# Kernel optimization log

Hardware: AMD Instinct MI355X
Metric: run time of the kernel (lower is better)

## Reference

```python
import jax, jax.numpy as jnp
import numpy as np

# ---------------- config (from ObjectDetector source) ----------------
B = 2; IMG = 224; STRIDE = 32; FH = IMG // STRIDE          # 7x7 feature map
C_FEAT = 1024
SIZES = (32., 64., 128., 256., 512.); RATIOS = (0.5, 1.0, 2.0)
A = len(SIZES) * len(RATIOS)                                # 15 anchors/loc
NA = FH * FH * A                                            # 735 anchors/img
PRE_NMS = min(1000, NA); POST_NMS = min(1000, NA)           # testing config
RPN_NMS_T = 0.7; RPN_MIN_SIZE = 1e-3
NUM_CLASSES = 37
ROI_OUT = 7; ROI_SR = 2; ROI_SCALE = 1.0 / STRIDE
REP = 1024
SCORE_T = 0.05; DET_NMS_T = 0.5; DETS_PER_IMG = 100
CAND_K = 2048            # candidate cap before final batched NMS
MIN_SIZE_DET = 1e-2
BBOX_CLIP = float(np.log(1000.0 / 16.0))


def make_anchors():
    scales = np.array(SIZES, np.float32); ratios = np.array(RATIOS, np.float32)
    h_r = np.sqrt(ratios); w_r = 1.0 / h_r
    ws = (w_r[:, None] * scales[None, :]).reshape(-1)
    hs = (h_r[:, None] * scales[None, :]).reshape(-1)
    base = np.round(np.stack([-ws, -hs, ws, hs], 1) / 2.0)   # [A,4]
    sy, sx = np.meshgrid(np.arange(FH) * STRIDE, np.arange(FH) * STRIDE, indexing='ij')
    shifts = np.stack([sx.reshape(-1), sy.reshape(-1), sx.reshape(-1), sy.reshape(-1)], 1).astype(np.float32)
    return jnp.asarray((shifts[:, None, :] + base[None, :, :]).reshape(-1, 4))  # [NA,4] (H,W,A)


def conv(x, w, b, stride=1, pad=0):
    y = jax.lax.conv_general_dilated(x, w, (stride, stride), [(pad, pad)] * 2,
                                     dimension_numbers=('NCHW', 'OIHW', 'NCHW'))
    return y + b[None, :, None, None]


def decode_boxes(deltas, boxes, weights):
    wx, wy, ww, wh = weights
    w = boxes[..., 2] - boxes[..., 0]; h = boxes[..., 3] - boxes[..., 1]
    cx = boxes[..., 0] + 0.5 * w; cy = boxes[..., 1] + 0.5 * h
    dx = deltas[..., 0] / wx; dy = deltas[..., 1] / wy
    dw = jnp.minimum(deltas[..., 2] / ww, BBOX_CLIP)
    dh = jnp.minimum(deltas[..., 3] / wh, BBOX_CLIP)
    pcx = dx * w + cx; pcy = dy * h + cy
    pw = jnp.exp(dw) * w; ph = jnp.exp(dh) * h
    return jnp.stack([pcx - 0.5 * pw, pcy - 0.5 * ph, pcx + 0.5 * pw, pcy + 0.5 * ph], -1)


def clip_boxes(b):
    x = jnp.clip(b[..., 0::2], 0.0, float(IMG)); y = jnp.clip(b[..., 1::2], 0.0, float(IMG))
    return jnp.stack([x[..., 0], y[..., 0], x[..., 1], y[..., 1]], -1)


def box_iou(a, b):
    area_a = (a[:, 2] - a[:, 0]) * (a[:, 3] - a[:, 1])
    area_b = (b[:, 2] - b[:, 0]) * (b[:, 3] - b[:, 1])
    lt = jnp.maximum(a[:, None, :2], b[None, :, :2])
    rb = jnp.minimum(a[:, None, 2:], b[None, :, 2:])
    wh = jnp.clip(rb - lt, 0.0, None)
    inter = wh[..., 0] * wh[..., 1]
    return inter / jnp.maximum(area_a[:, None] + area_b[None, :] - inter, 1e-9)


def nms_keep(boxes, scores, thresh):
    """Greedy NMS; returns keep mask in original order (fixed shapes)."""
    n = boxes.shape[0]
    order = jnp.argsort(-scores)
    iou = box_iou(*(jax.lax.stop_gradient(boxes[order]),) * 2)
    idx = jnp.arange(n)
    def body(i, keep):
        sup = (iou[i] > thresh) & (idx > i) & keep[i]
        return keep & ~sup
    keep_sorted = jax.lax.fori_loop(0, n, body, jnp.ones(n, bool))
    return jnp.zeros(n, bool).at[order].set(keep_sorted)


def rpn_filter_one(obj_logits, deltas, anchors):
    # obj_logits [NA], deltas [NA,4] (detached, as in torchvision RPN)
    top_v, top_i = jax.lax.top_k(obj_logits, PRE_NMS)
    boxes = clip_boxes(decode_boxes(deltas[top_i], anchors[top_i], (1., 1., 1., 1.)))
    prob = jax.nn.sigmoid(top_v)
    ws = boxes[:, 2] - boxes[:, 0]; hs = boxes[:, 3] - boxes[:, 1]
    prob = jnp.where((ws >= RPN_MIN_SIZE) & (hs >= RPN_MIN_SIZE), prob, -1.0)
    prob = jnp.where(nms_keep(boxes, prob, RPN_NMS_T), prob, -1.0)
    sv, si = jax.lax.top_k(prob, POST_NMS)
    return boxes[si], sv > 0.0


def bilinear(f_hwc, ys, xs):
    # torchvision roi_align bilinear sampling; f_hwc [H,W,C], ys/xs [R,O]
    H, W, _ = f_hwc.shape
    vy = (ys >= -1.0) & (ys <= H); vx = (xs >= -1.0) & (xs <= W)
    y = jnp.clip(ys, 0.0, None); x = jnp.clip(xs, 0.0, None)
    y0 = jnp.minimum(jnp.floor(y).astype(jnp.int32), H - 1)
    x0 = jnp.minimum(jnp.floor(x).astype(jnp.int32), W - 1)
    y1 = jnp.minimum(y0 + 1, H - 1); x1 = jnp.minimum(x0 + 1, W - 1)
    y = jnp.where(y0 == H - 1, y0.astype(y.dtype), y)
    x = jnp.where(x0 == W - 1, x0.astype(x.dtype), x)
    ly = y - y0; lx = x - x0; hy = 1.0 - ly; hx = 1.0 - lx
    g = lambda yi, xi: f_hwc[yi[:, :, None], xi[:, None, :]]   # [R,O,O,C]
    val = ((hy[:, :, None] * hx[:, None, :])[..., None] * g(y0, x0)
         + (hy[:, :, None] * lx[:, None, :])[..., None] * g(y0, x1)
         + (ly[:, :, None] * hx[:, None, :])[..., None] * g(y1, x0)
         + (ly[:, :, None] * lx[:, None, :])[..., None] * g(y1, x1))
    return val * (vy[:, :, None] & vx[:, None, :])[..., None]


def roi_align_one(feat_chw, rois):
    # feat [C,H,W], rois [R,4] -> [R,C,7,7]; output_size=7, sampling_ratio=2, scale=1/32
    f = jnp.transpose(feat_chw, (1, 2, 0))
    x1 = rois[:, 0] * ROI_SCALE; y1 = rois[:, 1] * ROI_SCALE
    rw = jnp.maximum(rois[:, 2] * ROI_SCALE - x1, 1.0)
    rh = jnp.maximum(rois[:, 3] * ROI_SCALE - y1, 1.0)
    bw = rw / ROI_OUT; bh = rh / ROI_OUT
    grid = jnp.arange(ROI_OUT, dtype=jnp.float32)
    acc = 0.0
    for iy in range(ROI_SR):
        ys = y1[:, None] + (grid[None, :] + (iy + 0.5) / ROI_SR) * bh[:, None]
        for ix in range(ROI_SR):
            xs = x1[:, None] + (grid[None, :] + (ix + 0.5) / ROI_SR) * bw[:, None]
            acc = acc + bilinear(f, ys, xs)
    return jnp.transpose(acc / (ROI_SR * ROI_SR), (0, 3, 1, 2))


def postprocess_one(logits, box_deltas, proposals, roi_valid):
    R = logits.shape[0]
    scores = jax.nn.softmax(logits, -1)
    boxes = clip_boxes(decode_boxes(box_deltas.reshape(R, NUM_CLASSES, 4),
                                    proposals[:, None, :], (10., 10., 5., 5.)))
    boxes = boxes[:, 1:, :].reshape(-1, 4)       # drop background class
    scores = jnp.where(roi_valid[:, None], scores[:, 1:], 0.0).reshape(-1)
    labels = jnp.broadcast_to(jnp.arange(1, NUM_CLASSES)[None, :], (R, NUM_CLASSES - 1)).reshape(-1)
    ws = boxes[:, 2] - boxes[:, 0]; hs = boxes[:, 3] - boxes[:, 1]
    ok = (ws >= MIN_SIZE_DET) & (hs >= MIN_SIZE_DET) & (scores > SCORE_T)
    cs, ci = jax.lax.top_k(jnp.where(ok, scores, -1.0), CAND_K)
    cb = boxes[ci]; cl = labels[ci]
    off = cl.astype(cb.dtype) * (IMG + 1.0)      # batched (per-class) NMS trick
    keep = nms_keep(cb + off[:, None], cs, DET_NMS_T)
    tv, ti = jax.lax.top_k(jnp.where(keep, cs, -1.0), DETS_PER_IMG)
    valid = tv > 0.0
    out_boxes = jnp.where(valid[:, None], cb[ti], 0.0)
    out_scores = jnp.where(valid, tv, 0.0)
    out_labels = jnp.where(valid, cl[ti], 0).astype(out_boxes.dtype)
    return jnp.concatenate([out_boxes, out_scores[:, None], out_labels[:, None]], -1)  # [100,6]


def forward(images, params, anchors):
    (bb_w, bb_b, rpn_w, rpn_b, cls_w, cls_b, reg_w, reg_b,
     fc1_w, fc1_b, fc2_w, fc2_b, clsp_w, clsp_b, boxp_w, boxp_b) = params
    Bn = images.shape[0]
    feats = jax.nn.relu(conv(images, bb_w, bb_b, stride=STRIDE))        # [B,1024,7,7]
    t = jax.nn.relu(conv(feats, rpn_w, rpn_b, stride=1, pad=1))
    obj = jnp.transpose(conv(t, cls_w, cls_b), (0, 2, 3, 1)).reshape(Bn, -1)            # [B,NA]
    reg = jnp.transpose(conv(t, reg_w, reg_b).reshape(Bn, A, 4, FH, FH),
                        (0, 3, 4, 1, 2)).reshape(Bn, -1, 4)                              # [B,NA,4]
    obj_d = jax.lax.stop_gradient(obj); reg_d = jax.lax.stop_gradient(reg)  # RPN detaches
    proposals, roi_valid = jax.vmap(lambda o, d: rpn_filter_one(o, d, anchors))(obj_d, reg_d)
    pooled = jax.vmap(roi_align_one)(feats, proposals)                  # [B,R,1024,7,7]
    x = pooled.reshape(Bn * POST_NMS, -1)
    x = jax.nn.relu(x @ fc1_w.T + fc1_b)
    x = jax.nn.relu(x @ fc2_w.T + fc2_b)
    logits = (x @ clsp_w.T + clsp_b).reshape(Bn, POST_NMS, NUM_CLASSES)
    bdelt = (x @ boxp_w.T + boxp_b).reshape(Bn, POST_NMS, NUM_CLASSES * 4)
    return jax.vmap(postprocess_one)(logits, bdelt, proposals, roi_valid)  # [B,100,6]


def setup_inputs() -> dict:
    key = jax.random.key(0)
    ks = jax.random.split(key, 10)
    w = lambda k, shape, s=0.02: jax.random.normal(k, shape, jnp.float32) * s
    return {
        'images': jax.random.uniform(ks[0], (B, 1, IMG, IMG), jnp.float32),
        'bb_w': w(ks[1], (C_FEAT, 1, STRIDE, STRIDE)), 'bb_b': jnp.zeros((C_FEAT,), jnp.float32),
        'rpn_w': w(ks[2], (C_FEAT, C_FEAT, 3, 3)), 'rpn_b': jnp.zeros((C_FEAT,), jnp.float32),
        'cls_w': w(ks[3], (A, C_FEAT, 1, 1)), 'cls_b': jnp.zeros((A,), jnp.float32),
        'reg_w': w(ks[4], (4 * A, C_FEAT, 1, 1)), 'reg_b': jnp.zeros((4 * A,), jnp.float32),
        'fc1_w': w(ks[5], (REP, C_FEAT * ROI_OUT * ROI_OUT), 0.005), 'fc1_b': jnp.zeros((REP,), jnp.float32),
        'fc2_w': w(ks[6], (REP, REP)), 'fc2_b': jnp.zeros((REP,), jnp.float32),
        'clsp_w': w(ks[7], (NUM_CLASSES, REP)), 'clsp_b': jnp.zeros((NUM_CLASSES,), jnp.float32),
        'boxp_w': w(ks[8], (NUM_CLASSES * 4, REP)), 'boxp_b': jnp.zeros((NUM_CLASSES * 4,), jnp.float32),
    }


def reference(images, bb_w, bb_b, rpn_w, rpn_b, cls_w, cls_b, reg_w, reg_b,
              fc1_w, fc1_b, fc2_w, fc2_b, clsp_w, clsp_b, boxp_w, boxp_b):
    anchors = make_anchors()
    params = (bb_w, bb_b, rpn_w, rpn_b, cls_w, cls_b, reg_w, reg_b,
              fc1_w, fc1_b, fc2_w, fc2_b, clsp_w, clsp_b, boxp_w, boxp_b)
    return forward(images, params, anchors)
```

## Files before the change

### kernel.cpp

```cpp
#include <hip/hip_runtime.h>
#include <math.h>

#define NANCH 735
#define NCAND 26460
#define NCANDP 26624
#define BBCLIP 4.135166556742356f
#define KF1 4864
#define KHALF 2432

typedef short bf16x8 __attribute__((ext_vector_type(8)));
typedef float f32x4 __attribute__((ext_vector_type(4)));

__device__ __forceinline__ unsigned short f2b(float f) {
  unsigned int u = __float_as_uint(f);
  unsigned int r = (u >> 16) & 1u;
  u += 0x7fffu + r;
  return (unsigned short)(u >> 16);
}

__device__ __forceinline__ void anchor_of(int i, float* o) {
  int pos = i / 15, a = i % 15;
  int iy = pos / 7, ix = pos % 7;
  int rr = a / 5, sc = a % 5;
  double ratio = (rr == 0) ? 0.5 : (rr == 1 ? 1.0 : 2.0);
  double scale = (double)(32 << sc);
  double hr = sqrt(ratio), wr = 1.0 / hr;
  double wsz = wr * scale, hsz = hr * scale;
  float bx1 = (float)rint(-wsz * 0.5), by1 = (float)rint(-hsz * 0.5);
  float bx2 = (float)rint(wsz * 0.5),  by2 = (float)rint(hsz * 0.5);
  float sx = (float)(ix * 32), sy = (float)(iy * 32);
  o[0] = sx + bx1; o[1] = sy + by1; o[2] = sx + bx2; o[3] = sy + by2;
}

__device__ __forceinline__ bool before_(float va, int ia, float vb, int ib) {
  return (va > vb) || (va == vb && ia < ib);
}

template<int NTOT, int NTH>
__device__ void bitonic_sort_sh(float* v, int* id) {
  const int t = threadIdx.x;
  for (int k = 2; k <= NTOT; k <<= 1) {
    for (int j = k >> 1; j > 0; j >>= 1) {
      for (int s = t; s < NTOT; s += NTH) {
        int p = s ^ j;
        if (p > s) {
          float v1 = v[s], v2 = v[p];
          int i1 = id[s], i2 = id[p];
          bool up = ((s & k) == 0);
          if (before_(v2, i2, v1, i1) == up) {
            v[s] = v2; id[s] = i2; v[p] = v1; id[p] = i1;
          }
        }
      }
      __syncthreads();
    }
  }
}

template<int NTOT, int NTH>
__device__ void bitonic_merge_sh(float* v, int* id) {
  const int t = threadIdx.x;
  for (int j = NTOT >> 1; j > 0; j >>= 1) {
    for (int s = t; s < NTOT; s += NTH) {
      int p = s ^ j;
      if (p > s) {
        float v1 = v[s], v2 = v[p];
        int i1 = id[s], i2 = id[p];
        if (before_(v2, i2, v1, i1)) {
          v[s] = v2; id[s] = i2; v[p] = v1; id[p] = i1;
        }
      }
    }
    __syncthreads();
  }
}

__global__ void k_im2col_bb(const float* __restrict__ images, unsigned short* __restrict__ patch) {
  int i = blockIdx.x * 256 + threadIdx.x;
  if (i >= 98 * 1024) return;
  int rowi = i >> 10, k = i & 1023;
  int b = rowi / 49, pos = rowi % 49;
  int oy = pos / 7, ox = pos % 7;
  int ky = k >> 5, kx = k & 31;
  patch[i] = f2b(images[((size_t)b * 224 + oy * 32 + ky) * 224 + ox * 32 + kx]);
}

__global__ void k_im2col_rpn(const unsigned short* __restrict__ bbh,
                             unsigned short* __restrict__ im2) {
  int i = blockIdx.x * 256 + threadIdx.x;
  if (i >= 98 * 9216) return;
  int rowi = i / 9216, k = i % 9216;
  int b = rowi / 49, pos = rowi % 49;
  int oy = pos / 7, ox = pos % 7;
  int ic = k / 9, kk = k % 9;
  int ky = kk / 3, kx = kk % 3;
  int y = oy + ky - 1, x = ox + kx - 1;
  unsigned short v = 0;
  if ((unsigned)y < 7u && (unsigned)x < 7u)
    v = bbh[((size_t)(b * 49 + y * 7 + x)) * 1024 + ic];
  im2[i] = v;
}

__global__ __launch_bounds__(256) void k_gemm_bf16(
    const unsigned short* __restrict__ A, int lda, int M,
    const unsigned short* __restrict__ B, int ldb,
    float* __restrict__ P, int N, int Kchunk,
    const int* __restrict__ nvalid)
{
  __shared__ __attribute__((aligned(16))) unsigned short As[2][128][40];
  __shared__ __attribute__((aligned(16))) unsigned short Bs[2][128][40];
  const int G = gridDim.x * gridDim.y * gridDim.z;
  int lid = blockIdx.x + gridDim.x * (blockIdx.y + gridDim.y * blockIdx.z);
  lid = (lid & 7) * (G >> 3) + (lid >> 3);
  const int bx = lid % gridDim.x;
  const int rest = lid / gridDim.x;
  const int by = rest % gridDim.y, bz = rest / gridDim.y;
  const int m0 = bx * 128, n0 = by * 128;
  if (nvalid) {
    int nv0 = nvalid[0], nv1 = nvalid[1];
    bool ok = (m0 < nv0) || ((m0 + 128 > NANCH) && (m0 < NANCH + nv1));
    if (!ok) return;
  }
  const int t = threadIdx.x;
  const int lane = t & 63, wid = t >> 6;
  const int wm = (wid >> 1) * 64, wn = (wid & 1) * 64;
  const size_t k0 = (size_t)bz * Kchunk;
  f32x4 acc[4][4];
#pragma unroll
  for (int i = 0; i < 4; ++i)
#pragma unroll
    for (int j = 0; j < 4; ++j) acc[i][j] = (f32x4){0.f, 0.f, 0.f, 0.f};
  const int r0 = t >> 2, c0 = (t & 3) * 8;
  const int fr = lane & 15, fk = (lane >> 4) * 8;
  const int gmA0 = m0 + r0, gmA1 = m0 + r0 + 64;
  const bool vA0 = gmA0 < M, vA1 = gmA1 < M;
  const unsigned short* pA0 = A + (size_t)gmA0 * lda + k0 + c0;
  const unsigned short* pA1 = A + (size_t)gmA1 * lda + k0 + c0;
  const unsigned short* pB0 = B + (size_t)(n0 + r0) * ldb + k0 + c0;
  const unsigned short* pB1 = B + (size_t)(n0 + r0 + 64) * ldb + k0 + c0;
  bf16x8 rA0 = {}, rA1 = {}, rB0, rB1;
  if (vA0) rA0 = *(const bf16x8*)pA0;
  if (vA1) rA1 = *(const bf16x8*)pA1;
  rB0 = *(const bf16x8*)pB0;
  rB1 = *(const bf16x8*)pB1;
  const int nt = Kchunk >> 5;
  int cur = 0;
  for (int it = 0; it < nt; ++it) {
    *(bf16x8*)&As[cur][r0][c0] = rA0;
    *(bf16x8*)&As[cur][r0 + 64][c0] = rA1;
    *(bf16x8*)&Bs[cur][r0][c0] = rB0;
    *(bf16x8*)&Bs[cur][r0 + 64][c0] = rB1;
    __syncthreads();
    if (it + 1 < nt) {
      size_t ofs = (size_t)(it + 1) * 32;
      rA0 = vA0 ? *(const bf16x8*)(pA0 + ofs) : (bf16x8){};
      rA1 = vA1 ? *(const bf16x8*)(pA1 + ofs) : (bf16x8){};
      rB0 = *(const bf16x8*)(pB0 + ofs);
      rB1 = *(const bf16x8*)(pB1 + ofs);
    }
    bf16x8 af[4], bg[4];
#pragma unroll
    for (int i = 0; i < 4; ++i) af[i] = *(const bf16x8*)&As[cur][wm + i * 16 + fr][fk];
#pragma unroll
    for (int j = 0; j < 4; ++j) bg[j] = *(const bf16x8*)&Bs[cur][wn + j * 16 + fr][fk];
#pragma unroll
    for (int i = 0; i < 4; ++i)
#pragma unroll
      for (int j = 0; j < 4; ++j)
        acc[i][j] = __builtin_amdgcn_mfma_f32_16x16x32_bf16(af[i], bg[j], acc[i][j], 0, 0, 0);
    cur ^= 1;
  }
  float* Pp = P + (size_t)bz * M * N;
#pragma unroll
  for (int i = 0; i < 4; ++i) {
#pragma unroll
    for (int r = 0; r < 4; ++r) {
      int gm = m0 + wm + i * 16 + (lane >> 4) * 4 + r;
      if (gm < M) {
#pragma unroll
        for (int j = 0; j < 4; ++j)
          Pp[(size_t)gm * N + n0 + wn + j * 16 + (lane & 15)] = acc[i][j][r];
      }
    }
  }
}

__global__ __launch_bounds__(256) void k_gemm_mb(
    const unsigned short* __restrict__ A,
    const unsigned short* __restrict__ W1p,
    unsigned short* __restrict__ Bmat)
{
  __shared__ __attribute__((aligned(16))) unsigned short As[2][128][40];
  __shared__ __attribute__((aligned(16))) unsigned short Bs[2][128][40];
  __shared__ unsigned short tile[98][130];
  const int G = gridDim.x * gridDim.y * gridDim.z;
  int lid = blockIdx.x + gridDim.x * (blockIdx.y + gridDim.y * blockIdx.z);
  lid = (lid & 7) * (G >> 3) + (lid >> 3);
  const int rest = lid;
  const int by = rest % gridDim.y, p = rest / gridDim.y;
  const int n0 = by * 128;
  const int M = 98;
  const unsigned short* B = W1p + (size_t)p * 1048576;
  const int t = threadIdx.x;
  const int lane = t & 63, wid = t >> 6;
  const int wm = (wid >> 1) * 64, wn = (wid & 1) * 64;
  f32x4 acc[4][4];
#pragma unroll
  for (int i = 0; i < 4; ++i)
#pragma unroll
    for (int j = 0; j < 4; ++j) acc[i][j] = (f32x4){0.f, 0.f, 0.f, 0.f};
  const int r0 = t >> 2, c0 = (t & 3) * 8;
  const int fr = lane & 15, fk = (lane >> 4) * 8;
  int gA0 = r0; if (gA0 >= M) gA0 = M - 1;
  int gA1 = r0 + 64; if (gA1 >= M) gA1 = M - 1;
  const unsigned short* pA0 = A + (size_t)gA0 * 1024 + c0;
  const unsigned short* pA1 = A + (size_t)gA1 * 1024 + c0;
  const unsigned short* pB0 = B + (size_t)(n0 + r0) * 1024 + c0;
  const unsigned short* pB1 = B + (size_t)(n0 + r0 + 64) * 1024 + c0;
  bf16x8 rA0 = *(const bf16x8*)pA0;
  bf16x8 rA1 = *(const bf16x8*)pA1;
  bf16x8 rB0 = *(const bf16x8*)pB0;
  bf16x8 rB1 = *(const bf16x8*)pB1;
  const int nt = 1024 >> 5;
  int cur = 0;
  for (int it = 0; it < nt; ++it) {
    *(bf16x8*)&As[cur][r0][c0] = rA0;
    *(bf16x8*)&As[cur][r0 + 64][c0] = rA1;
    *(bf16x8*)&Bs[cur][r0][c0] = rB0;
    *(bf16x8*)&Bs[cur][r0 + 64][c0] = rB1;
    __syncthreads();
    if (it + 1 < nt) {
      size_t ofs = (size_t)(it + 1) * 32;
      rA0 = *(const bf16x8*)(pA0 + ofs);
      rA1 = *(const bf16x8*)(pA1 + ofs);
      rB0 = *(const bf16x8*)(pB0 + ofs);
      rB1 = *(const bf16x8*)(pB1 + ofs);
    }
    bf16x8 af[4], bg[4];
#pragma unroll
    for (int i = 0; i < 4; ++i) af[i] = *(const bf16x8*)&As[cur][wm + i * 16 + fr][fk];
#pragma unroll
    for (int j = 0; j < 4; ++j) bg[j] = *(const bf16x8*)&Bs[cur][wn + j * 16 + fr][fk];
#pragma unroll
    for (int i = 0; i < 4; ++i)
#pragma unroll
      for (int j = 0; j < 4; ++j)
        acc[i][j] = __builtin_amdgcn_mfma_f32_16x16x32_bf16(af[i], bg[j], acc[i][j], 0, 0, 0);
    cur ^= 1;
  }
  __syncthreads();
#pragma unroll
  for (int i = 0; i < 4; ++i) {
#pragma unroll
    for (int r = 0; r < 4; ++r) {
      int gm = wm + i * 16 + (lane >> 4) * 4 + r;
      if (gm < M) {
#pragma unroll
        for (int j = 0; j < 4; ++j)
          tile[gm][wn + j * 16 + (lane & 15)] = f2b(acc[i][j][r]);
      }
    }
  }
  __syncthreads();
  {
    int nl = t >> 1, b2 = t & 1;
    unsigned short* dst = Bmat + (size_t)(n0 + nl) * KF1 + b2 * KHALF + p * 49;
    for (int qq = 0; qq < 49; ++qq) dst[qq] = tile[b2 * 49 + qq][nl];
  }
  if (p == 0) {
    for (int j2 = t; j2 < 128 * 62; j2 += 256) {
      int nl = j2 / 62, e = j2 % 62;
      int bb = e >= 31 ? 1 : 0;
      int col = bb * KHALF + 2401 + (e - bb * 31);
      Bmat[(size_t)(n0 + nl) * KF1 + col] = 0;
    }
  }
}

__global__ __launch_bounds__(256) void k_gbuild(const float* __restrict__ props,
                                                unsigned short* __restrict__ Gmat)
{
#pragma clang fp contract(off)
  int rg = blockIdx.x;
  int b = rg / NANCH;
  __shared__ float g[KF1];
  int t = threadIdx.x;
  for (int j = t; j < KF1; j += 256) g[j] = 0.f;
  __syncthreads();
  if (t < 49) {
    const float* roi = props + (size_t)rg * 4;
    int p = t, oy = p / 7, ox = p % 7;
    float x1 = roi[0] * 0.03125f, y1 = roi[1] * 0.03125f;
    float rw = fmaxf(roi[2] * 0.03125f - x1, 1.f);
    float rh = fmaxf(roi[3] * 0.03125f - y1, 1.f);
    float bw = rw / 7.f, bh = rh / 7.f;
    float* gb = g + b * KHALF + p * 49;
    for (int iy = 0; iy < 2; ++iy) {
      for (int ix = 0; ix < 2; ++ix) {
        float ys = y1 + ((float)oy + ((float)iy + 0.5f) * 0.5f) * bh;
        float xs = x1 + ((float)ox + ((float)ix + 0.5f) * 0.5f) * bw;
        bool vy = (ys >= -1.f) && (ys <= 7.f);
        bool vx = (xs >= -1.f) && (xs <= 7.f);
        float yc = fmaxf(ys, 0.f), xc = fmaxf(xs, 0.f);
        int y0 = min((int)floorf(yc), 6), x0 = min((int)floorf(xc), 6);
        int y1i = min(y0 + 1, 6), x1i = min(x0 + 1, 6);
        if (y0 == 6) yc = 6.f;
        if (x0 == 6) xc = 6.f;
        float ly = yc - (float)y0, lx = xc - (float)x0;
        float hy = 1.f - ly, hx = 1.f - lx;
        float vm = (vy && vx) ? 0.25f : 0.f;
        gb[y0 * 7 + x0]   += hy * hx * vm;
        gb[y0 * 7 + x1i]  += hy * lx * vm;
        gb[y1i * 7 + x0]  += ly * hx * vm;
        gb[y1i * 7 + x1i] += ly * lx * vm;
      }
    }
  }
  __syncthreads();
  unsigned short* Gr = Gmat + (size_t)rg * KF1;
  for (int j = t; j < KF1; j += 256) Gr[j] = f2b(g[j]);
}

__global__ void k_reduce(const float* __restrict__ P, float* __restrict__ dst,
                         unsigned short* __restrict__ dst16,
                         int S, int M, int N, const float* __restrict__ bias, int flags)
{
  size_t i = (size_t)blockIdx.x * 256 + threadIdx.x;
  size_t tot = (size_t)M * N;
  if (i >= tot) return;
  float v = (flags & 1) ? 0.f : dst[i];
  for (int s = 0; s < S; ++s) v += P[(size_t)s * tot + i];
  if (flags & 2) v += bias[i % (size_t)N];
  if (flags & 4) v = fmaxf(v, 0.f);
  if (!(flags & 16)) dst[i] = v;
  if (flags & 8) dst16[i] = f2b(v);
}

__global__ void k_f2b3(const float* __restrict__ s1, unsigned short* __restrict__ d1,
                       const float* __restrict__ s2, unsigned short* __restrict__ d2,
                       const float* __restrict__ s3, unsigned short* __restrict__ d3,
                       const float* __restrict__ cw, const float* __restrict__ bw,
                       unsigned short* __restrict__ d4)
{
  int i = (blockIdx.x * 256 + threadIdx.x) * 4;
  const float* s; unsigned short* d; int off;
  if (i < 1048576) { s = s1; d = d1; off = i; }
  else if (i < 2097152) { s = s2; d = d2; off = i - 1048576; }
  else if (i < 11534336) { s = s3; d = d3; off = i - 2097152; }
  else if (i < 11796480) {
    int off4 = i - 11534336;
    int row = off4 >> 10, col = off4 & 1023;
    ushort4 o;
    if (row < 37) {
      float4 v = *(const float4*)(cw + (size_t)row * 1024 + col);
      o.x = f2b(v.x); o.y = f2b(v.y); o.z = f2b(v.z); o.w = f2b(v.w);
    } else if (row < 185) {
      float4 v = *(const float4*)(bw + (size_t)(row - 37) * 1024 + col);
      o.x = f2b(v.x); o.y = f2b(v.y); o.z = f2b(v.z); o.w = f2b(v.w);
    } else {
      o.x = 0; o.y = 0; o.z = 0; o.w = 0;
    }
    *(ushort4*)(d4 + off4) = o;
    return;
  }
  else return;
  float4 v = *(const float4*)(s + off);
  ushort4 o;
  o.x = f2b(v.x); o.y = f2b(v.y); o.z = f2b(v.z); o.w = f2b(v.w);
  *(ushort4*)(d + off) = o;
}

__global__ __launch_bounds__(256) void k_w1perm2(const float* __restrict__ w,
                                                 unsigned short* __restrict__ o)
{
  __shared__ unsigned short tile[128 * 50];
  const int n = blockIdx.x, ct = blockIdx.y;
  const float* src = w + (size_t)n * 50176 + (size_t)ct * 128 * 49;
  const int t = threadIdx.x;
  for (int i = t; i < 6272; i += 256) {
    int cl = i / 49, p = i % 49;
    tile[cl * 50 + p] = f2b(src[i]);
  }
  __syncthreads();
  for (int j = t; j < 6272; j += 256) {
    int p = j >> 7, cl = j & 127;
    o[((size_t)p * 1024 + n) * 1024 + (size_t)ct * 128 + cl] = tile[cl * 50 + p];
  }
}

__global__ __launch_bounds__(256) void k_rpn_head(
    const float* __restrict__ tmn, const float* __restrict__ cls_w,
    const float* __restrict__ cls_b, const float* __restrict__ reg_w,
    const float* __restrict__ reg_b, float* __restrict__ obj, float* __restrict__ reg)
{
  int blk = blockIdx.x;
  __shared__ float col[1024];
  const float* row = tmn + (size_t)blk * 1024;
  for (int i = threadIdx.x; i < 1024; i += 256) col[i] = row[i];
  __syncthreads();
  int b = blk / 49, pos = blk % 49;
  for (int o = threadIdx.x; o < 75; o += 256) {
    const float* w = (o < 15) ? (cls_w + (size_t)o * 1024) : (reg_w + (size_t)(o - 15) * 1024);
    float s = 0.f;
    for (int k = 0; k < 1024; ++k) s = fmaf(col[k], w[k], s);
    if (o < 15) {
      obj[(size_t)b * NANCH + pos * 15 + o] = s + cls_b[o];
    } else {
      int c = o - 15, a = c >> 2, d = c & 3;
      reg[((size_t)b * NANCH + pos * 15 + a) * 4 + d] = s + reg_b[c];
    }
  }
}

__global__ __launch_bounds__(1024) void k_rpn_prep(
    const float* __restrict__ obj, const float* __restrict__ reg,
    float* __restrict__ bxp, float* __restrict__ pnms)
{
#pragma clang fp contract(off)
  const int b = blockIdx.x, t = threadIdx.x;
  __shared__ float sval[1024];
  __shared__ float vo1[1024];
  __shared__ int o1a[1024];
  __shared__ int wtv[16];
  __shared__ int wti[16];
  sval[t] = (t < NANCH) ? obj[(size_t)b * NANCH + t] : -INFINITY;
  __syncthreads();
  {
    float v = sval[t];
    int rank = 0;
    for (int j = 0; j < NANCH; ++j) {
      float u = sval[j];
      rank += (u > v) || (u == v && j < t);
    }
    if (t < NANCH) { vo1[rank] = v; o1a[rank] = t; }
  }
  __syncthreads();
  float x1 = 0.f, y1 = 0.f, x2 = 0.f, y2 = 0.f, prob = -1.f;
  bool flag = false;
  if (t < NANCH) {
    int ai = o1a[t];
    const float* d = reg + ((size_t)b * NANCH + ai) * 4;
    float an[4];
    anchor_of(ai, an);
    float aw = an[2] - an[0], ah = an[3] - an[1];
    float acx = an[0] + 0.5f * aw, acy = an[1] + 0.5f * ah;
    float dw = fminf(d[2], BBCLIP), dh = fminf(d[3], BBCLIP);
    float pcx = d[0] * aw + acx, pcy = d[1] * ah + acy;
    float pw = expf(dw) * aw, ph = expf(dh) * ah;
    x1 = pcx - 0.5f * pw; y1 = pcy - 0.5f * ph;
    x2 = pcx + 0.5f * pw; y2 = pcy + 0.5f * ph;
    x1 = fminf(fmaxf(x1, 0.f), 224.f);
    y1 = fminf(fmaxf(y1, 0.f), 224.f);
    x2 = fminf(fmaxf(x2, 0.f), 224.f);
    y2 = fminf(fmaxf(y2, 0.f), 224.f);
    flag = (x2 - x1 >= 1e-3f) && (y2 - y1 >= 1e-3f);
    prob = 1.f / (1.f + expf(-vo1[t]));
  }
  bool iflag = (t < NANCH) && !flag;
  unsigned long long balv = __ballot(flag);
  unsigned long long bali = __ballot(iflag);
  int lane = t & 63, w = t >> 6;
  if (lane == 0) { wtv[w] = __popcll(balv); wti[w] = __popcll(bali); }
  __syncthreads();
  int nval = 0, basev = 0, basei = 0;
  for (int k = 0; k < 16; ++k) {
    int cv = wtv[k], ci = wti[k];
    nval += cv;
    if (k < w) { basev += cv; basei += ci; }
  }
  if (t < NANCH) {
    unsigned long long lm = (1ull << lane) - 1;
    int pos = flag ? (basev + __popcll(balv & lm))
                   : (nval + basei + __popcll(bali & lm));
    float* o = bxp + ((size_t)b * NANCH + pos) * 4;
    o[0] = x1; o[1] = y1; o[2] = x2; o[3] = y2;
    pnms[(size_t)b * NANCH + pos] = flag ? prob : -1.f;
  }
}

__global__ __launch_bounds__(256) void k_rpn_mask(
    const float* __restrict__ bxp, unsigned long long* __restrict__ rmask)
{
#pragma clang fp contract(off)
  int blk = blockIdx.x;
  int b = blk / 35;
  int row = (blk % 35) * 21 + (int)(threadIdx.x / 12);
  int w = threadIdx.x % 12;
  if (threadIdx.x >= 252 || row >= NANCH) return;
  const float* a = bxp + ((size_t)b * NANCH + row) * 4;
  float a0 = a[0], a1 = a[1], a2 = a[2], a3 = a[3];
  float aarea = (a2 - a0) * (a3 - a1);
  int l0 = w * 64;
  int l1 = (l0 + 64 < NANCH) ? l0 + 64 : NANCH;
  int ls = (l0 > row + 1) ? l0 : row + 1;
  unsigned long long bits = 0ull;
  for (int l = ls; l < l1; ++l) {
    const float* q = bxp + ((size_t)b * NANCH + l) * 4;
    float b0 = q[0], b1 = q[1], b2 = q[2], b3 = q[3];
    float barea = (b2 - b0) * (b3 - b1);
    float ix1 = fmaxf(a0, b0), iy1 = fmaxf(a1, b1);
    float ix2 = fminf(a2, b2), iy2 = fminf(a3, b3);
    float iw = fmaxf(ix2 - ix1, 0.f), ih = fmaxf(iy2 - iy1, 0.f);
    float inter = iw * ih;
    float iou = inter / fmaxf(aarea + barea - inter, 1e-9f);
    if (iou > 0.7f) bits |= 1ull << (l & 63);
  }
  rmask[((size_t)b * NANCH + row) * 12 + w] = bits;
}

__global__ __launch_bounds__(1024) void k_rpn_fin(
    const float* __restrict__ bxp, const float* __restrict__ pnms,
    const unsigned long long* __restrict__ rmask,
    float* __restrict__ props, int* __restrict__ meta)
{
  const int b = blockIdx.x, t = threadIdx.x;
  __shared__ unsigned long long smask[NANCH * 12];
  __shared__ float sp[1024];
  __shared__ unsigned long long keepw[12];
  __shared__ int wtot[16];
  for (int i = t; i < NANCH * 12; i += 1024)
    smask[i] = rmask[(size_t)b * NANCH * 12 + i];
  sp[t] = (t < NANCH) ? pnms[(size_t)b * NANCH + t] : -1.f;
  __syncthreads();
  if (t < 64) {
    unsigned long long kl = (t < 12) ? ~0ull : 0ull;
    for (int i = 0; i < NANCH; ++i) {
      unsigned long long kw = __shfl(kl, i >> 6);
      unsigned long long m = (t < 12) ? smask[i * 12 + t] : 0ull;
      bool on = (kw >> (i & 63)) & 1ull;
      kl &= on ? ~m : ~0ull;
    }
    if (t < 12) keepw[t] = kl;
  }
  __syncthreads();
  bool flag = false;
  if (t < NANCH) {
    bool kp = (keepw[t >> 6] >> (t & 63)) & 1ull;
    flag = kp && (sp[t] > 0.f);
  }
  unsigned long long bal = __ballot(flag);
  int lane = t & 63, w = t >> 6;
  if (lane == 0) wtot[w] = __popcll(bal);
  __syncthreads();
  int base = 0, tot = 0;
  for (int k = 0; k < 16; ++k) { int c = wtot[k]; if (k < w) base += c; tot += c; }
  if (flag) {
    int pos = base + __popcll(bal & ((1ull << lane) - 1));
    const float* src = bxp + ((size_t)b * NANCH + t) * 4;
    float* o = props + ((size_t)b * NANCH + pos) * 4;
    o[0] = src[0]; o[1] = src[1]; o[2] = src[2]; o[3] = src[3];
  }
  if (t == 0) meta[b] = tot;
}

__global__ void k_cand(const float* __restrict__ P, const float* __restrict__ cb_,
                       const float* __restrict__ bb_, const float* __restrict__ props,
                       const int* __restrict__ meta,
                       float* __restrict__ cscore, float* __restrict__ cbox)
{
#pragma clang fp contract(off)
  int rg = blockIdx.x * blockDim.x + threadIdx.x;
  if (rg >= 2 * NANCH) return;
  int b = rg / NANCH, r = rg % NANCH;
  float* cs = cscore + (size_t)b * NCANDP;
  float* cbx = cbox + (size_t)b * NCANDP * 4;
  int base = r * 36;
  if (r >= meta[b]) {
    for (int j = 0; j < 36; ++j) {
      cs[base + j] = -1.f;
      float* q = cbx + (size_t)(base + j) * 4;
      q[0] = 0.f; q[1] = 0.f; q[2] = 0.f; q[3] = 0.f;
    }
    return;
  }
  const float* p0 = P + (size_t)rg * 256;
  const float* p1 = P + 1470ull * 256 + (size_t)rg * 256;
  float lg[37];
  for (int c = 0; c < 37; ++c) lg[c] = p0[c] + p1[c] + cb_[c];
  float mx = lg[0];
  for (int c = 1; c < 37; ++c) mx = fmaxf(mx, lg[c]);
  float sum = 0.f;
  for (int c = 0; c < 37; ++c) sum += expf(lg[c] - mx);
  const float* roi = props + (size_t)rg * 4;
  float rw = roi[2] - roi[0], rh = roi[3] - roi[1];
  float rcx = roi[0] + 0.5f * rw, rcy = roi[1] + 0.5f * rh;
  for (int c = 1; c < 37; ++c) {
    float d0 = p0[37 + c * 4]     + p1[37 + c * 4]     + bb_[c * 4];
    float d1 = p0[37 + c * 4 + 1] + p1[37 + c * 4 + 1] + bb_[c * 4 + 1];
    float d2 = p0[37 + c * 4 + 2] + p1[37 + c * 4 + 2] + bb_[c * 4 + 2];
    float d3 = p0[37 + c * 4 + 3] + p1[37 + c * 4 + 3] + bb_[c * 4 + 3];
    float dx = d0 / 10.f, dy = d1 / 10.f;
    float dw = fminf(d2 / 5.f, BBCLIP), dh = fminf(d3 / 5.f, BBCLIP);
    float pcx = dx * rw + rcx, pcy = dy * rh + rcy;
    float pw = expf(dw) * rw, ph = expf(dh) * rh;
    float x1 = pcx - 0.5f * pw, y1 = pcy - 0.5f * ph;
    float x2 = pcx + 0.5f * pw, y2 = pcy + 0.5f * ph;
    x1 = fminf(fmaxf(x1, 0.f), 224.f);
    y1 = fminf(fmaxf(y1, 0.f), 224.f);
    x2 = fminf(fmaxf(x2, 0.f), 224.f);
    y2 = fminf(fmaxf(y2, 0.f), 224.f);
    float sc = expf(lg[c] - mx) / sum;
    bool ok = ((x2 - x1) >= 1e-2f) && ((y2 - y1) >= 1e-2f) && (sc > 0.05f);
    cs[base + c - 1] = ok ? sc : -1.f;
    float* q = cbx + (size_t)(base + c - 1) * 4;
    q[0] = x1; q[1] = y1; q[2] = x2; q[3] = y2;
  }
}

__global__ __launch_bounds__(1024) void k_top2048(
    const float* __restrict__ cscore,
    float* __restrict__ sel_score, int* __restrict__ sel_cidx,
    int* __restrict__ meta)
{
  const int b = blockIdx.x, t = threadIdx.x;
  __shared__ float Lv[2048]; __shared__ int Li[2048];
  __shared__ float Cv[2048]; __shared__ int Ci[2048];
  __shared__ int cnt;
  const float* cs = cscore + (size_t)b * NCANDP;
  if (t == 0) cnt = 0;
  __syncthreads();
  for (int gi = t; gi < NCAND; gi += 1024) {
    float v = cs[gi];
    if (v > 0.f) {
      int p = atomicAdd(&cnt, 1);
      if (p < 2048) { Cv[p] = v; Ci[p] = gi; }
    }
  }
  __syncthreads();
  int npos = cnt;
  if (npos <= 2048) {
    for (int h = 0; h < 2; ++h) {
      int p = h * 1024 + t;
      if (p < npos) {
        float v = Cv[p]; int id = Ci[p];
        int rank = 0;
        for (int j = 0; j < npos; ++j) {
          float u = Cv[j]; int ju = Ci[j];
          rank += (u > v) || (u == v && ju < id);
        }
        sel_score[b * 2048 + rank] = v;
        sel_cidx[b * 2048 + rank] = id;
      }
      if (p >= npos && p < 2048) {
        sel_score[b * 2048 + p] = -1.f;
        sel_cidx[b * 2048 + p] = 0;
      }
    }
    if (t == 0) meta[2 + b] = npos;
    return;
  }
  for (int chunk = 0; chunk < 13; ++chunk) {
    for (int s = t; s < 2048; s += 1024) {
      int gi = chunk * 2048 + s;
      Cv[s] = (gi < NCAND) ? cs[gi] : -INFINITY;
      Ci[s] = gi;
    }
    __syncthreads();
    bitonic_sort_sh<2048, 1024>(Cv, Ci);
    if (chunk == 0) {
      for (int s = t; s < 2048; s += 1024) { Lv[s] = Cv[s]; Li[s] = Ci[s]; }
      __syncthreads();
    } else {
      for (int s = t; s < 2048; s += 1024) {
        float cv = Cv[2047 - s]; int ci = Ci[2047 - s];
        if (before_(cv, ci, Lv[s], Li[s])) { Lv[s] = cv; Li[s] = ci; }
      }
      __syncthreads();
      bitonic_merge_sh<2048, 1024>(Lv, Li);
    }
  }
  for (int s = t; s < 2048; s += 1024) {
    sel_score[b * 2048 + s] = Lv[s];
    sel_cidx[b * 2048 + s] = Li[s];
  }
  if (t == 0) meta[2 + b] = 2048;
}

__global__ void k_detmask(const int* __restrict__ sel_cidx,
                          const float* __restrict__ cbox,
                          const int* __restrict__ meta,
                          unsigned long long* __restrict__ dmask)
{
#pragma clang fp contract(off)
  int blk = blockIdx.x;
  int b = blk >> 8, row0 = (blk & 255) * 8;
  int npos = meta[2 + b];
  if (row0 >= npos) return;
  int t = threadIdx.x;
  int i = row0 + (t >> 5), w = t & 31;
  if (i >= npos) return;
  int ci = sel_cidx[b * 2048 + i];
  const float* bp = cbox + ((size_t)b * NCANDP + ci) * 4;
  float off = (float)(ci % 36 + 1) * 225.f;
  float a0 = bp[0] + off, a1 = bp[1] + off, a2 = bp[2] + off, a3 = bp[3] + off;
  float aarea = (a2 - a0) * (a3 - a1);
  unsigned long long bits = 0ull;
  int l0 = w * 64;
  int l1 = (l0 + 64 < npos) ? l0 + 64 : npos;
  int ls = (l0 > i + 1) ? l0 : i + 1;
  for (int l = ls; l < l1; ++l) {
    int cl = sel_cidx[b * 2048 + l];
    const float* q = cbox + ((size_t)b * NCANDP + cl) * 4;
    float o2 = (float)(cl % 36 + 1) * 225.f;
    float b0 = q[0] + o2, b1 = q[1] + o2, b2 = q[2] + o2, b3 = q[3] + o2;
    float barea = (b2 - b0) * (b3 - b1);
    float ix1 = fmaxf(a0, b0), iy1 = fmaxf(a1, b1);
    float ix2 = fminf(a2, b2), iy2 = fminf(a3, b3);
    float iw = fmaxf(ix2 - ix1, 0.f), ih = fmaxf(iy2 - iy1, 0.f);
    float inter = iw * ih;
    float iou = inter / fmaxf(aarea + barea - inter, 1e-9f);
    if (iou > 0.5f) bits |= 1ull << (l & 63);
  }
  dmask[((size_t)b * 2048 + i) * 32 + w] = bits;
}

__global__ __launch_bounds__(1024) void k_final(
    const float* __restrict__ sel_score, const int* __restrict__ sel_cidx,
    const float* __restrict__ cbox, const unsigned long long* __restrict__ dmask,
    const int* __restrict__ meta, float* __restrict__ out)
{
  const int b = blockIdx.x, t = threadIdx.x;
  __shared__ unsigned long long keepw[32];
  __shared__ float sv[2048];
  __shared__ float kv[2048]; __shared__ int ks[2048];
  __shared__ int wtot[32];
  int npos = meta[2 + b];
  for (int h = 0; h < 2; ++h) {
    int s = h * 1024 + t;
    sv[s] = sel_score[b * 2048 + s];
  }
  __syncthreads();
  if (t < 64) {
    unsigned long long kl = (t < 32) ? ~0ull : 0ull;
    for (int i = 0; i < npos; ++i) {
      unsigned long long kw = __shfl(kl, i >> 6);
      unsigned long long m = (t < 32) ? dmask[((size_t)b * 2048 + i) * 32 + t] : 0ull;
      bool on = (kw >> (i & 63)) & 1ull;
      kl &= on ? ~m : ~0ull;
    }
    if (t < 32) keepw[t] = kl;
  }
  __syncthreads();
  const int lane = t & 63, w = t >> 6;
  int s0 = t;
  bool f0 = ((keepw[s0 >> 6] >> (s0 & 63)) & 1ull) && (sv[s0] > 0.f);
  unsigned long long bal0 = __ballot(f0);
  if (lane == 0) wtot[w] = __popcll(bal0);
  int s1 = 1024 + t;
  bool f1 = ((keepw[s1 >> 6] >> (s1 & 63)) & 1ull) && (sv[s1] > 0.f);
  unsigned long long bal1 = __ballot(f1);
  if (lane == 0) wtot[16 + w] = __popcll(bal1);
  __syncthreads();
  int nk = 0, base0 = 0, base1 = 0;
  for (int k = 0; k < 32; ++k) {
    int c = wtot[k];
    if (k < w) base0 += c;
    if (k < 16 + w) base1 += c;
    nk += c;
  }
  int p0 = -1, p1 = -1;
  if (f0) { p0 = base0 + __popcll(bal0 & ((1ull << lane) - 1)); kv[p0] = sv[s0]; ks[p0] = s0; }
  if (f1) { p1 = base1 + __popcll(bal1 & ((1ull << lane) - 1)); kv[p1] = sv[s1]; ks[p1] = s1; }
  __syncthreads();
  if (f0) {
    float v = sv[s0]; int rank = 0;
    for (int j = 0; j < nk; ++j) { float u = kv[j]; int ju = ks[j]; rank += (u > v) || (u == v && ju < s0); }
    if (rank < 100) {
      int ci = sel_cidx[b * 2048 + s0];
      const float* bp = cbox + ((size_t)b * NCANDP + ci) * 4;
      float* o = out + ((size_t)b * 100 + rank) * 6;
      o[0] = bp[0]; o[1] = bp[1]; o[2] = bp[2]; o[3] = bp[3];
      o[4] = v; o[5] = (float)(ci % 36 + 1);
    }
  }
  if (f1) {
    float v = sv[s1]; int rank = 0;
    for (int j = 0; j < nk; ++j) { float u = kv[j]; int ju = ks[j]; rank += (u > v) || (u == v && ju < s1); }
    if (rank < 100) {
      int ci = sel_cidx[b * 2048 + s1];
      const float* bp = cbox + ((size_t)b * NCANDP + ci) * 4;
      float* o = out + ((size_t)b * 100 + rank) * 6;
      o[0] = bp[0]; o[1] = bp[1]; o[2] = bp[2]; o[3] = bp[3];
      o[4] = v; o[5] = (float)(ci % 36 + 1);
    }
  }
  if (t < 100 && t >= nk) {
    float* o = out + ((size_t)b * 100 + t) * 6;
    o[0] = 0.f; o[1] = 0.f; o[2] = 0.f; o[3] = 0.f; o[4] = 0.f; o[5] = 0.f;
  }
}

extern "C" void kernel_launch(void* const* d_in, const int* in_sizes, int n_in,
                              void* d_out, int out_size, void* d_ws, size_t ws_size,
                              hipStream_t stream)
{
  (void)in_sizes; (void)n_in; (void)out_size; (void)ws_size;
  const float* images = (const float*)d_in[0];
  const float* bb_w   = (const float*)d_in[1];
  const float* bb_b   = (const float*)d_in[2];
  const float* rpn_w  = (const float*)d_in[3];
  const float* rpn_b  = (const float*)d_in[4];
  const float* cls_w  = (const float*)d_in[5];
  const float* cls_b  = (const float*)d_in[6];
  const float* reg_w  = (const float*)d_in[7];
  const float* reg_b  = (const float*)d_in[8];
  const float* fc1_w  = (const float*)d_in[9];
  const float* fc1_b  = (const float*)d_in[10];
  const float* fc2_w  = (const float*)d_in[11];
  const float* fc2_b  = (const float*)d_in[12];
  const float* clsp_w = (const float*)d_in[13];
  const float* clsp_b = (const float*)d_in[14];
  const float* boxp_w = (const float*)d_in[15];
  const float* boxp_b = (const float*)d_in[16];
  float* out = (float*)d_out;
  char* ws = (char*)d_ws;

  size_t off = 0;
  auto alloc = [&](size_t bytes) -> size_t {
    size_t o = off; off = (off + bytes + 255) & ~(size_t)255; return o;
  };
  size_t o_patch = alloc(98ull * 1024 * 2);
  size_t o_bbC   = alloc(98ull * 1024 * 4);
  size_t o_bbh   = alloc(98ull * 1024 * 2);
  size_t o_t     = alloc(98ull * 1024 * 4);
  size_t o_im2   = alloc(98ull * 9216 * 2);
  size_t o_obj   = alloc(1470ull * 4);
  size_t o_reg   = alloc(1470ull * 16);
  size_t o_props = alloc(1470ull * 16);
  size_t o_bxp   = alloc(1470ull * 16);
  size_t o_pnms  = alloc(1470ull * 4);
  size_t o_rm    = alloc(1470ull * 12 * 8);
  size_t o_meta  = alloc(256);
  size_t o_y1    = alloc(1470ull * 1024 * 4);
  size_t o_y2    = alloc(1470ull * 1024 * 4);
  size_t o_cs    = alloc(2ull * NCANDP * 4);
  size_t o_cb    = alloc(2ull * NCANDP * 16);
  size_t o_ss    = alloc(2ull * 2048 * 4);
  size_t o_sc    = alloc(2ull * 2048 * 4);
  size_t o_dm    = alloc(2ull * 2048 * 32 * 8);
  size_t o_w0b   = alloc(1048576ull * 2);
  size_t o_w3b   = alloc(9437184ull * 2);
  size_t o_w1p   = alloc(51380224ull * 2);
  size_t o_bmat  = alloc(1024ull * KF1 * 2);
  size_t o_gmat  = alloc(1470ull * KF1 * 2);
  size_t o_w2b   = alloc(1048576ull * 2);
  size_t o_hwb   = alloc(256ull * 1024 * 2);
  size_t o_y1b   = alloc(1470ull * 1024 * 2);
  size_t o_y2b   = alloc(1470ull * 1024 * 2);
  size_t o_P     = alloc(32ull * 98 * 1024 * 4 > 4ull * 1470 * 1024 * 4
                         ? 32ull * 98 * 1024 * 4 : 4ull * 1470 * 1024 * 4);

  unsigned short* patchb = (unsigned short*)(ws + o_patch);
  float* bbC   = (float*)(ws + o_bbC);
  unsigned short* bbh = (unsigned short*)(ws + o_bbh);
  float* tb    = (float*)(ws + o_t);
  unsigned short* im2b = (unsigned short*)(ws + o_im2);
  float* objb  = (float*)(ws + o_obj);
  float* regb  = (float*)(ws + o_reg);
  float* props = (float*)(ws + o_props);
  float* bxp   = (float*)(ws + o_bxp);
  float* pnms  = (float*)(ws + o_pnms);
  unsigned long long* rmb = (unsigned long long*)(ws + o_rm);
  int*   meta  = (int*)(ws + o_meta);
  float* y1    = (float*)(ws + o_y1);
  float* csb   = (float*)(ws + o_cs);
  float* cbb   = (float*)(ws + o_cb);
  float* ssb   = (float*)(ws + o_ss);
  int*   scb   = (int*)(ws + o_sc);
  unsigned long long* dmb = (unsigned long long*)(ws + o_dm);
  unsigned short* w0b = (unsigned short*)(ws + o_w0b);
  unsigned short* w3b = (unsigned short*)(ws + o_w3b);
  unsigned short* w1p = (unsigned short*)(ws + o_w1p);
  unsigned short* bmat = (unsigned short*)(ws + o_bmat);
  unsigned short* gmat = (unsigned short*)(ws + o_gmat);
  unsigned short* w2b = (unsigned short*)(ws + o_w2b);
  unsigned short* hwb = (unsigned short*)(ws + o_hwb);
  unsigned short* y1b = (unsigned short*)(ws + o_y1b);
  unsigned short* y2b = (unsigned short*)(ws + o_y2b);
  float* Pb    = (float*)(ws + o_P);

  k_w1perm2<<<dim3(1024, 8), 256, 0, stream>>>(fc1_w, w1p);
  k_f2b3<<<11520, 256, 0, stream>>>(fc2_w, w2b, bb_w, w0b, rpn_w, w3b, clsp_w, boxp_w, hwb);
  k_im2col_bb<<<392, 256, 0, stream>>>(images, patchb);
  k_gemm_bf16<<<dim3(1, 8, 8), 256, 0, stream>>>(patchb, 1024, 98, w0b, 1024, Pb, 1024, 128, nullptr);
  k_reduce<<<392, 256, 0, stream>>>(Pb, bbC, bbh, 8, 98, 1024, bb_b, 31);
  k_gemm_mb<<<dim3(1, 8, 49), 256, 0, stream>>>(bbh, w1p, bmat);
  k_im2col_rpn<<<3528, 256, 0, stream>>>(bbh, im2b);
  k_gemm_bf16<<<dim3(1, 8, 32), 256, 0, stream>>>(im2b, 9216, 98, w3b, 9216, Pb, 1024, 288, nullptr);
  k_reduce<<<392, 256, 0, stream>>>(Pb, tb, nullptr, 32, 98, 1024, rpn_b, 7);
  k_rpn_head<<<98, 256, 0, stream>>>(tb, cls_w, cls_b, reg_w, reg_b, objb, regb);
  k_rpn_prep<<<2, 1024, 0, stream>>>(objb, regb, bxp, pnms);
  k_rpn_mask<<<70, 256, 0, stream>>>(bxp, rmb);
  k_rpn_fin<<<2, 1024, 0, stream>>>(bxp, pnms, rmb, props, meta);
  k_gbuild<<<1470, 256, 0, stream>>>(props, gmat);
  k_gemm_bf16<<<dim3(12, 8, 4), 256, 0, stream>>>(gmat, KF1, 1470, bmat, KF1, Pb, 1024, 1216, meta);
  k_reduce<<<5880, 256, 0, stream>>>(Pb, y1, y1b, 4, 1470, 1024, fc1_b, 31);
  k_gemm_bf16<<<dim3(12, 8, 2), 256, 0, stream>>>(y1b, 1024, 1470, w2b, 1024, Pb, 1024, 512, meta);
  k_reduce<<<5880, 256, 0, stream>>>(Pb, y1, y2b, 2, 1470, 1024, fc2_b, 31);
  k_gemm_bf16<<<dim3(12, 2, 2), 256, 0, stream>>>(y2b, 1024, 1470, hwb, 1024, Pb, 256, 512, meta);
  k_cand<<<6, 256, 0, stream>>>(Pb, clsp_b, boxp_b, props, meta, csb, cbb);
  k_top2048<<<2, 1024, 0, stream>>>(csb, ssb, scb, meta);
  k_detmask<<<512, 256, 0, stream>>>(scb, cbb, meta, dmb);
  k_final<<<2, 1024, 0, stream>>>(ssb, scb, cbb, dmb, meta, out);
}
```

Baseline: 455.1 us.

## Split fc1 ROI GEMM per image to skip the zero half of K

Each image's ROIs are padded to 768 rows so that every 128-row tile belongs to a single image. The per-image gather matrix now holds only that image's K half (2432 columns), and the GEMM shifts the B pointer by image. This halves the K work and gather-matrix traffic of the fc1 GEMM, since the other image's half was all zeros, and it halves the split-K partials to reduce. The cost is some padded rows (1536 vs 1470), a changed row indexing in the downstream kernels, and a new lower clamp on the bilinear indices.

```diff
diff --git a/kernel.cpp b/kernel.cpp
--- a/kernel.cpp
+++ b/kernel.cpp
@@ -7,6 +7,8 @@
 #define BBCLIP 4.135166556742356f
 #define KF1 4864
 #define KHALF 2432
+#define MROW 768
+#define MTOT 1536
 
 typedef short bf16x8 __attribute__((ext_vector_type(8)));
 typedef float f32x4 __attribute__((ext_vector_type(4)));
@@ -105,7 +107,7 @@
     const unsigned short* __restrict__ A, int lda, int M,
     const unsigned short* __restrict__ B, int ldb,
     float* __restrict__ P, int N, int Kchunk,
-    const int* __restrict__ nvalid)
+    const int* __restrict__ nvalid, int Msplit, int boff)
 {
   __shared__ __attribute__((aligned(16))) unsigned short As[2][128][40];
   __shared__ __attribute__((aligned(16))) unsigned short Bs[2][128][40];
@@ -117,9 +119,10 @@
   const int by = rest % gridDim.y, bz = rest / gridDim.y;
   const int m0 = bx * 128, n0 = by * 128;
   if (nvalid) {
-    int nv0 = nvalid[0], nv1 = nvalid[1];
-    bool ok = (m0 < nv0) || ((m0 + 128 > NANCH) && (m0 < NANCH + nv1));
-    if (!ok) return;
+    int img = (Msplit && m0 >= Msplit) ? 1 : 0;
+    int lm = m0 - img * Msplit;
+    if (lm >= nvalid[img]) return;
+    B += (size_t)img * boff;
   }
   const int t = threadIdx.x;
   const int lane = t & 63, wid = t >> 6;
@@ -282,19 +285,20 @@
 {
 #pragma clang fp contract(off)
   int rg = blockIdx.x;
-  int b = rg / NANCH;
-  __shared__ float g[KF1];
+  int b = rg / MROW, r = rg % MROW;
+  __shared__ float g[KHALF];
   int t = threadIdx.x;
-  for (int j = t; j < KF1; j += 256) g[j] = 0.f;
+  for (int j = t; j < KHALF; j += 256) g[j] = 0.f;
   __syncthreads();
   if (t < 49) {
-    const float* roi = props + (size_t)rg * 4;
+    int pr = b * NANCH + r; if (pr > 2 * NANCH - 1) pr = 2 * NANCH - 1;
+    const float* roi = props + (size_t)pr * 4;
     int p = t, oy = p / 7, ox = p % 7;
     float x1 = roi[0] * 0.03125f, y1 = roi[1] * 0.03125f;
     float rw = fmaxf(roi[2] * 0.03125f - x1, 1.f);
     float rh = fmaxf(roi[3] * 0.03125f - y1, 1.f);
     float bw = rw / 7.f, bh = rh / 7.f;
-    float* gb = g + b * KHALF + p * 49;
+    float* gb = g + p * 49;
     for (int iy = 0; iy < 2; ++iy) {
       for (int ix = 0; ix < 2; ++ix) {
         float ys = y1 + ((float)oy + ((float)iy + 0.5f) * 0.5f) * bh;
@@ -302,7 +306,7 @@
         bool vy = (ys >= -1.f) && (ys <= 7.f);
         bool vx = (xs >= -1.f) && (xs <= 7.f);
         float yc = fmaxf(ys, 0.f), xc = fmaxf(xs, 0.f);
-        int y0 = min((int)floorf(yc), 6), x0 = min((int)floorf(xc), 6);
+        int y0 = min(max((int)floorf(yc), 0), 6), x0 = min(max((int)floorf(xc), 0), 6);
         int y1i = min(y0 + 1, 6), x1i = min(x0 + 1, 6);
         if (y0 == 6) yc = 6.f;
         if (x0 == 6) xc = 6.f;
@@ -317,8 +321,8 @@
     }
   }
   __syncthreads();
-  unsigned short* Gr = Gmat + (size_t)rg * KF1;
-  for (int j = t; j < KF1; j += 256) Gr[j] = f2b(g[j]);
+  unsigned short* Gr = Gmat + (size_t)rg * KHALF;
+  for (int j = t; j < KHALF; j += 256) Gr[j] = f2b(g[j]);
 }
 
 __global__ void k_reduce(const float* __restrict__ P, float* __restrict__ dst,
@@ -573,8 +577,9 @@
     }
     return;
   }
-  const float* p0 = P + (size_t)rg * 256;
-  const float* p1 = P + 1470ull * 256 + (size_t)rg * 256;
+  int row = b * MROW + r;
+  const float* p0 = P + (size_t)row * 256;
+  const float* p1 = P + (size_t)MTOT * 256 + (size_t)row * 256;
   float lg[37];
   for (int c = 0; c < 37; ++c) lg[c] = p0[c] + p1[c] + cb_[c];
   float mx = lg[0];
@@ -831,8 +836,7 @@
   size_t o_pnms  = alloc(1470ull * 4);
   size_t o_rm    = alloc(1470ull * 12 * 8);
   size_t o_meta  = alloc(256);
-  size_t o_y1    = alloc(1470ull * 1024 * 4);
-  size_t o_y2    = alloc(1470ull * 1024 * 4);
+  size_t o_y1    = alloc((size_t)MTOT * 1024 * 4);
   size_t o_cs    = alloc(2ull * NCANDP * 4);
   size_t o_cb    = alloc(2ull * NCANDP * 16);
   size_t o_ss    = alloc(2ull * 2048 * 4);
@@ -842,13 +846,13 @@
   size_t o_w3b   = alloc(9437184ull * 2);
   size_t o_w1p   = alloc(51380224ull * 2);
   size_t o_bmat  = alloc(1024ull * KF1 * 2);
-  size_t o_gmat  = alloc(1470ull * KF1 * 2);
+  size_t o_gmat  = alloc((size_t)MTOT * KHALF * 2);
   size_t o_w2b   = alloc(1048576ull * 2);
   size_t o_hwb   = alloc(256ull * 1024 * 2);
-  size_t o_y1b   = alloc(1470ull * 1024 * 2);
-  size_t o_y2b   = alloc(1470ull * 1024 * 2);
-  size_t o_P     = alloc(32ull * 98 * 1024 * 4 > 4ull * 1470 * 1024 * 4
-                         ? 32ull * 98 * 1024 * 4 : 4ull * 1470 * 1024 * 4);
+  size_t o_y1b   = alloc((size_t)MTOT * 1024 * 2);
+  size_t o_y2b   = alloc((size_t)MTOT * 1024 * 2);
+  size_t o_P     = alloc(32ull * 98 * 1024 * 4 > 2ull * MTOT * 1024 * 4
+                         ? 32ull * 98 * 1024 * 4 : 2ull * MTOT * 1024 * 4);
 
   unsigned short* patchb = (unsigned short*)(ws + o_patch);
   float* bbC   = (float*)(ws + o_bbC);
@@ -882,22 +886,22 @@
   k_w1perm2<<<dim3(1024, 8), 256, 0, stream>>>(fc1_w, w1p);
   k_f2b3<<<11520, 256, 0, stream>>>(fc2_w, w2b, bb_w, w0b, rpn_w, w3b, clsp_w, boxp_w, hwb);
   k_im2col_bb<<<392, 256, 0, stream>>>(images, patchb);
-  k_gemm_bf16<<<dim3(1, 8, 8), 256, 0, stream>>>(patchb, 1024, 98, w0b, 1024, Pb, 1024, 128, nullptr);
+  k_gemm_bf16<<<dim3(1, 8, 8), 256, 0, stream>>>(patchb, 1024, 98, w0b, 1024, Pb, 1024, 128, nullptr, 0, 0);
   k_reduce<<<392, 256, 0, stream>>>(Pb, bbC, bbh, 8, 98, 1024, bb_b, 31);
   k_gemm_mb<<<dim3(1, 8, 49), 256, 0, stream>>>(bbh, w1p, bmat);
   k_im2col_rpn<<<3528, 256, 0, stream>>>(bbh, im2b);
-  k_gemm_bf16<<<dim3(1, 8, 32), 256, 0, stream>>>(im2b, 9216, 98, w3b, 9216, Pb, 1024, 288, nullptr);
+  k_gemm_bf16<<<dim3(1, 8, 32), 256, 0, stream>>>(im2b, 9216, 98, w3b, 9216, Pb, 1024, 288, nullptr, 0, 0);
   k_reduce<<<392, 256, 0, stream>>>(Pb, tb, nullptr, 32, 98, 1024, rpn_b, 7);
   k_rpn_head<<<98, 256, 0, stream>>>(tb, cls_w, cls_b, reg_w, reg_b, objb, regb);
   k_rpn_prep<<<2, 1024, 0, stream>>>(objb, regb, bxp, pnms);
   k_rpn_mask<<<70, 256, 0, stream>>>(bxp, rmb);
   k_rpn_fin<<<2, 1024, 0, stream>>>(bxp, pnms, rmb, props, meta);
-  k_gbuild<<<1470, 256, 0, stream>>>(props, gmat);
-  k_gemm_bf16<<<dim3(12, 8, 4), 256, 0, stream>>>(gmat, KF1, 1470, bmat, KF1, Pb, 1024, 1216, meta);
-  k_reduce<<<5880, 256, 0, stream>>>(Pb, y1, y1b, 4, 1470, 1024, fc1_b, 31);
-  k_gemm_bf16<<<dim3(12, 8, 2), 256, 0, stream>>>(y1b, 1024, 1470, w2b, 1024, Pb, 1024, 512, meta);
-  k_reduce<<<5880, 256, 0, stream>>>(Pb, y1, y2b, 2, 1470, 1024, fc2_b, 31);
-  k_gemm_bf16<<<dim3(12, 2, 2), 256, 0, stream>>>(y2b, 1024, 1470, hwb, 1024, Pb, 256, 512, meta);
+  k_gbuild<<<MTOT, 256, 0, stream>>>(props, gmat);
+  k_gemm_bf16<<<dim3(12, 8, 2), 256, 0, stream>>>(gmat, KHALF, MTOT, bmat, KF1, Pb, 1024, 1216, meta, MROW, KHALF);
+  k_reduce<<<6144, 256, 0, stream>>>(Pb, y1, y1b, 2, MTOT, 1024, fc1_b, 31);
+  k_gemm_bf16<<<dim3(12, 8, 2), 256, 0, stream>>>(y1b, 1024, MTOT, w2b, 1024, Pb, 1024, 512, meta, MROW, 0);
+  k_reduce<<<6144, 256, 0, stream>>>(Pb, y1, y2b, 2, MTOT, 1024, fc2_b, 31);
+  k_gemm_bf16<<<dim3(12, 2, 2), 256, 0, stream>>>(y2b, 1024, MTOT, hwb, 1024, Pb, 256, 512, meta, MROW, 0);
   k_cand<<<6, 256, 0, stream>>>(Pb, clsp_b, boxp_b, props, meta, csb, cbb);
   k_top2048<<<2, 1024, 0, stream>>>(csb, ssb, scb, meta);
   k_detmask<<<512, 256, 0, stream>>>(scb, cbb, meta, dmb);
```

Result: no change. 447.9 us (-1.6%).
